# Optimization experiments

Measured on AMD Instinct MI355X. Metric: run time of the kernel, lower is better.

The kernel has to match this reference:

```python
import jax, jax.numpy as jnp
import numpy as np

NS = 50000   # sentence (src) nodes, unit==1
NW = 50000   # word (dst) nodes, unit==0
E = 1600000  # sw edges
IN_DIM = 128
OUT_DIM = 64


def setup_inputs() -> dict:
    key = jax.random.key(0)
    k1, k2, k3, k4, k5, k6 = jax.random.split(key, 6)
    return {
        "h": jax.random.normal(k1, (NS, IN_DIM), dtype=jnp.float32),
        "W_fc": jax.random.normal(k2, (IN_DIM, OUT_DIM), dtype=jnp.float32) * 0.05,
        "w_attn": jax.random.normal(k3, (2 * OUT_DIM, 1), dtype=jnp.float32) * 0.05,
        "weight": jax.random.uniform(k4, (E,), dtype=jnp.float32),
        "src_idx": jax.random.randint(k5, (E,), 0, NS, dtype=jnp.int32),
        "dst_idx": jax.random.randint(k6, (E,), 0, NW, dtype=jnp.int32),
    }


def reference(h, W_fc, w_attn, weight, src_idx, dst_idx):
    # z = fc(h) on source (sentence) nodes only; dst (word) nodes have z == 0 in DGL
    z = h @ W_fc                                   # [NS, OUT_DIM]
    zs = z[src_idx]                                # [E, OUT_DIM] gather src features
    # attn_fc(cat(z_src, z_dst)) with z_dst == 0 -> only first half of w_attn acts
    wa_src = w_attn[:OUT_DIM, 0]                   # [OUT_DIM]
    e = jax.nn.leaky_relu(zs @ wa_src)             # [E], slope 0.01 (torch default)
    e = weight * e                                 # tfidf edge weight scaling
    # edge-softmax per destination node (segment softmax over ragged mailbox)
    m = jax.ops.segment_max(e, dst_idx, num_segments=NW)          # [NW]
    m = jnp.where(jnp.isfinite(m), m, 0.0)                        # empty nodes
    ex = jnp.exp(e - m[dst_idx])                                  # [E]
    den = jax.ops.segment_sum(ex, dst_idx, num_segments=NW)       # [NW]
    alpha = ex / jnp.where(den == 0.0, 1.0, den)[dst_idx]         # [E]
    # weighted scatter-sum of neighbor features into dst nodes
    out = jax.ops.segment_sum(alpha[:, None] * zs, dst_idx, num_segments=NW)
    return out                                     # [NW, OUT_DIM]
```

## Files before the change

### kernel.cpp

```cpp
#include <hip/hip_runtime.h>
#include <hip/hip_fp16.h>
#include <math.h>

#define NS_ 50000
#define NW_ 50000
#define IN_DIM_ 128
#define OUT_DIM_ 64

#define NSLAB 512
#define NB 1563
#define CAPS 1280
#define CAPP 2304

typedef _Float16 h16x8 __attribute__((ext_vector_type(8)));
typedef float f32x4 __attribute__((ext_vector_type(4)));

__device__ inline float leaky01(float x) { return x > 0.0f ? x : 0.01f * x; }

__global__ __launch_bounds__(256) void prep_kernel(const float* __restrict__ Wfc,
                                                   const float* __restrict__ w_attn,
                                                   __half* __restrict__ W16f,
                                                   float* __restrict__ wv128) {
    int tid = threadIdx.x;
    for (int i = tid; i < IN_DIM_ * OUT_DIM_; i += 256) {
        int k = i >> 6, c = i & 63;
        int ni = c >> 4, c16 = c & 15, kstep = k >> 5, ks = (k & 31) >> 3, el = k & 7;
        W16f[(((ni * 4 + kstep) * 64) + ks * 16 + c16) * 8 + el] = __float2half(Wfc[i]);
    }
    if (tid < IN_DIM_) {
        float s = 0.f;
        for (int c = 0; c < OUT_DIM_; ++c) s += Wfc[tid * OUT_DIM_ + c] * w_attn[c];
        wv128[tid] = s;
    }
}

__global__ __launch_bounds__(256) void fc_kernel(const float* __restrict__ h,
                                                 const __half* __restrict__ W16f,
                                                 const float* __restrict__ wv128,
                                                 __half* __restrict__ z16,
                                                 float* __restrict__ t) {
    __shared__ __align__(16) __half Afrag[8192];
    __shared__ float ztile[64][68];
    int tid = threadIdx.x;
    int lane = tid & 63;
    int wv = tid >> 6;
    int row0 = blockIdx.x * 64;

    int k0 = (tid & 31) * 4;
    float4 wvv = *(const float4*)(wv128 + k0);
    int kstep = k0 >> 5, ks = (k0 & 31) >> 3, el = k0 & 7;
#pragma unroll
    for (int iter = 0; iter < 8; ++iter) {
        int r = (tid >> 5) + iter * 8;
        int row = row0 + r;
        float4 hv = (row < NS_) ? *(const float4*)(h + (size_t)row * IN_DIM_ + k0)
                                : make_float4(0.f, 0.f, 0.f, 0.f);
        int slot = ((r >> 4) * 4 + kstep) * 64 + ks * 16 + (r & 15);
        int slw = slot ^ ((slot >> 4) & 7);
        __half2 lo = __floats2half2_rn(hv.x, hv.y);
        __half2 hi = __floats2half2_rn(hv.z, hv.w);
        uint2 pk = make_uint2(*(unsigned*)&lo, *(unsigned*)&hi);
        *(uint2*)(&Afrag[slw * 8 + el]) = pk;
        float pt = hv.x * wvv.x + hv.y * wvv.y + hv.z * wvv.z + hv.w * wvv.w;
        pt += __shfl_down(pt, 16, 64);
        pt += __shfl_down(pt, 8, 64);
        pt += __shfl_down(pt, 4, 64);
        pt += __shfl_down(pt, 2, 64);
        pt += __shfl_down(pt, 1, 64);
        if ((tid & 31) == 0 && row < NS_) t[row] = pt;
    }
    __syncthreads();

    h16x8 af[4];
#pragma unroll
    for (int kst = 0; kst < 4; ++kst) {
        int s = (wv * 4 + kst) * 64 + lane;
        int sr = s ^ ((s >> 4) & 7);
        af[kst] = *(const h16x8*)(&Afrag[sr * 8]);
    }
#pragma unroll
    for (int ni = 0; ni < 4; ++ni) {
        f32x4 acc = {0.f, 0.f, 0.f, 0.f};
#pragma unroll
        for (int kst = 0; kst < 4; ++kst) {
            h16x8 bf = *(const h16x8*)(W16f + ((size_t)(ni * 4 + kst) * 64 + lane) * 8);
            acc = __builtin_amdgcn_mfma_f32_16x16x32_f16(af[kst], bf, acc, 0, 0, 0);
        }
        int col = ni * 16 + (lane & 15);
        int rb = wv * 16 + (lane >> 4) * 4;
        ztile[rb + 0][col] = acc[0];
        ztile[rb + 1][col] = acc[1];
        ztile[rb + 2][col] = acc[2];
        ztile[rb + 3][col] = acc[3];
    }
    __syncthreads();

    int nrows = NS_ - row0; if (nrows > 64) nrows = 64;
    for (int j = tid; j < 64 * 32; j += 256) {
        int r = j >> 5, c0 = (j & 31) * 2;
        if (r < nrows) {
            __half2 hp = __floats2half2_rn(ztile[r][c0], ztile[r][c0 + 1]);
            *(__half2*)(z16 + (size_t)(row0 + r) * OUT_DIM_ + c0) = hp;
        }
    }
}

__global__ __launch_bounds__(1024) void partition_kernel(const float* __restrict__ weight,
                                                         const int* __restrict__ src,
                                                         const int* __restrict__ dst,
                                                         const float* __restrict__ t,
                                                         unsigned* __restrict__ meta_sb,
                                                         int2* __restrict__ edata,
                                                         int E, int slab_e) {
    __shared__ int hist[NB];
    __shared__ int cur[NB];
    __shared__ int wsum[16];
    int tid = threadIdx.x;
    int lane = tid & 63;
    int wv = tid >> 6;
    int s = blockIdx.x;
    int e0 = s * slab_e;
    int e1 = e0 + slab_e; if (e1 > E) e1 = E;
    int cnt = e1 - e0;

    for (int i = tid; i < NB; i += 1024) hist[i] = 0;
    __syncthreads();

    float exr0 = 0, exr1 = 0, exr2 = 0, exr3 = 0;
    int mr0 = 0, mr1 = 0, mr2 = 0, mr3 = 0;
#define PART_LOAD(P, EXR, MR)                                              \
    {                                                                      \
        int i = tid + (P) * 1024;                                          \
        if (i < cnt) {                                                     \
            int e = e0 + i;                                                \
            int sr = src[e];                                               \
            int d = dst[e];                                                \
            float ev = weight[e] * leaky01(t[sr]);                         \
            EXR = __expf(ev);                                              \
            MR = sr | ((d & 31) << 16) | ((d >> 5) << 21);                 \
            atomicAdd(&hist[d >> 5], 1);                                   \
        }                                                                  \
    }
    PART_LOAD(0, exr0, mr0)
    PART_LOAD(1, exr1, mr1)
    PART_LOAD(2, exr2, mr2)
    PART_LOAD(3, exr3, mr3)
#undef PART_LOAD
    __syncthreads();

    int i0 = 2 * tid, i1 = 2 * tid + 1;
    int h0 = (i0 < NB) ? hist[i0] : 0;
    int h1 = (i1 < NB) ? hist[i1] : 0;
    int pairv = h0 + h1;
    int incl = pairv;
#pragma unroll
    for (int off = 1; off < 64; off <<= 1) {
        int u = __shfl_up(incl, off, 64);
        if (lane >= off) incl += u;
    }
    if (lane == 63) wsum[wv] = incl;
    __syncthreads();
    int woff = 0;
    for (int w = 0; w < wv; ++w) woff += wsum[w];
    incl += woff;
    int base = incl - pairv;
    if (i0 < NB) {
        cur[i0] = base;
        meta_sb[(size_t)s * NB + i0] = ((unsigned)h0 << 16) | (unsigned)base;
    }
    if (i1 < NB) {
        int b1 = base + h0;
        cur[i1] = b1;
        meta_sb[(size_t)s * NB + i1] = ((unsigned)h1 << 16) | (unsigned)b1;
    }
    __syncthreads();

#define PART_STORE(P, EXR, MR)                                             \
    {                                                                      \
        int i = tid + (P) * 1024;                                          \
        if (i < cnt) {                                                     \
            int b = ((unsigned)MR) >> 21;                                  \
            int pos = atomicAdd(&cur[b], 1);                               \
            edata[e0 + pos] = make_int2(__float_as_int(EXR), MR & 0x1FFFFF); \
        }                                                                  \
    }
    PART_STORE(0, exr0, mr0)
    PART_STORE(1, exr1, mr1)
    PART_STORE(2, exr2, mr2)
    PART_STORE(3, exr3, mr3)
#undef PART_STORE
}

__global__ __launch_bounds__(256) void meta_transpose_kernel(const unsigned* __restrict__ meta,
                                                             unsigned* __restrict__ metaT) {
    __shared__ unsigned tile[64][65];
    int b0 = blockIdx.x * 64;
    int s0 = blockIdx.y * 64;
    int tx = threadIdx.x & 63, ty = threadIdx.x >> 6;
    for (int r = ty; r < 64; r += 4) {
        int b = b0 + tx;
        tile[r][tx] = (b < NB) ? meta[(size_t)(s0 + r) * NB + b] : 0u;
    }
    __syncthreads();
    for (int r = ty; r < 64; r += 4) {
        int b = b0 + r;
        if (b < NB) metaT[(size_t)b * NSLAB + s0 + tx] = tile[tx][r];
    }
}

__global__ __launch_bounds__(512) void aggregate_kernel(const unsigned* __restrict__ metaT,
                                                        const int2* __restrict__ edata,
                                                        const __half* __restrict__ z16,
                                                        float* __restrict__ out,
                                                        int slab_e) {
    __shared__ int2 sbuf[CAPS];
    __shared__ int2 sorted[CAPP];
    __shared__ unsigned short soff[NSLAB];
    __shared__ int arr[NSLAB + 1];
    __shared__ int wsum[8];
    __shared__ float dden[32];
    __shared__ int dcnt[32];
    __shared__ int dbase[33];

    int orig = blockIdx.x;
    {
        const int nwg = NB, nx = 8;
        int q = nwg / nx, r = nwg % nx;
        int xcd = orig % nx, idx = orig / nx;
        orig = (xcd < r) ? xcd * (q + 1) + idx : r * (q + 1) + (xcd - r) * q + idx;
    }
    int b = orig;
    int tid = threadIdx.x;
    int lane = tid & 63;
    int wv = tid >> 6;

    int cntv;
    {
        unsigned mv = metaT[(size_t)b * NSLAB + tid];
        soff[tid] = (unsigned short)(mv & 0xFFFFu);
        cntv = (int)(mv >> 16);
    }
    if (tid < 32) { dden[tid] = 0.0f; dcnt[tid] = 0; }
    for (int i = tid; i < CAPP; i += 512) sorted[i] = make_int2(0, 0);

    int incl = cntv;
#pragma unroll
    for (int off = 1; off < 64; off <<= 1) {
        int u = __shfl_up(incl, off, 64);
        if (lane >= off) incl += u;
    }
    if (lane == 63) wsum[wv] = incl;
    __syncthreads();
    int woff = 0;
    for (int w = 0; w < wv; ++w) woff += wsum[w];
    incl += woff;
    arr[tid + 1] = incl;
    if (tid == 0) arr[0] = 0;
    __syncthreads();

    int total = arr[NSLAB];
    if (total > CAPS) total = CAPS;

    int gid = tid >> 1, l2 = tid & 1;
    for (int s = gid; s < NSLAB; s += 256) {
        int base = arr[s];
        int len = arr[s + 1] - base;
        int so = (int)soff[s];
        for (int j = l2; j < len; j += 2) {
            int p = base + j;
            if (p < CAPS) {
                int2 e = edata[(size_t)s * slab_e + so + j];
                sbuf[p] = e;
                int d5 = (e.y >> 16) & 31;
                atomicAdd(&dcnt[d5], 1);
                atomicAdd(&dden[d5], __int_as_float(e.x));
            }
        }
    }
    __syncthreads();

    if (tid < 32) {
        int v = dcnt[tid];
        int pv = (v + 31) & ~31;
        int iv = pv;
#pragma unroll
        for (int off = 1; off < 32; off <<= 1) {
            int u = __shfl_up(iv, off, 64);
            if (tid >= off) iv += u;
        }
        dbase[tid + 1] = iv;
        dcnt[tid] = iv - pv;
        if (tid == 0) dbase[0] = 0;
    }
    __syncthreads();

    for (int k = tid; k < total; k += 512) {
        int2 e = sbuf[k];
        int d5 = (e.y >> 16) & 31;
        int pos = atomicAdd(&dcnt[d5], 1);
        if (pos < CAPP) sorted[pos] = e;
    }
    __syncthreads();

    int qg = lane >> 4;
    int dl = lane & 15;
    const unsigned short* z16u = (const unsigned short*)z16;
    for (int q = 0; q < 4; ++q) {
        int d5 = wv * 4 + q;
        int d = b * 32 + d5;
        if (d >= NW_) continue;
        int a0 = dbase[d5];
        int npad = dbase[d5 + 1] - a0;
        float dn = dden[d5];
        float invdn = (dn > 0.0f) ? 1.0f / dn : 0.0f;
        float c0 = 0.f, c1 = 0.f, c2 = 0.f, c3 = 0.f;
        for (int j = 0; j < npad; j += 32) {
            int2 ee[8];
#pragma unroll
            for (int u = 0; u < 8; ++u) ee[u] = sorted[a0 + j + u * 4 + qg];
            uint2 zz[8];
#pragma unroll
            for (int u = 0; u < 8; ++u) {
                int srcr = ee[u].y & 0xFFFF;
                zz[u] = *(const uint2*)(z16u + (size_t)srcr * 64 + dl * 4);
            }
#pragma unroll
            for (int u = 0; u < 8; ++u) {
                float ex = __int_as_float(ee[u].x);
                __half2 p0 = *(__half2*)&zz[u].x;
                __half2 p1 = *(__half2*)&zz[u].y;
                c0 = fmaf(ex, __low2float(p0), c0);
                c1 = fmaf(ex, __high2float(p0), c1);
                c2 = fmaf(ex, __low2float(p1), c2);
                c3 = fmaf(ex, __high2float(p1), c3);
            }
        }
        c0 += __shfl_xor(c0, 16, 64); c1 += __shfl_xor(c1, 16, 64);
        c2 += __shfl_xor(c2, 16, 64); c3 += __shfl_xor(c3, 16, 64);
        c0 += __shfl_xor(c0, 32, 64); c1 += __shfl_xor(c1, 32, 64);
        c2 += __shfl_xor(c2, 32, 64); c3 += __shfl_xor(c3, 32, 64);
        if (lane < 16) {
            float4 st = make_float4(c0 * invdn, c1 * invdn, c2 * invdn, c3 * invdn);
            *(float4*)(out + (size_t)d * OUT_DIM_ + lane * 4) = st;
        }
    }
}

extern "C" void kernel_launch(void* const* d_in, const int* in_sizes, int n_in,
                              void* d_out, int out_size, void* d_ws, size_t ws_size,
                              hipStream_t stream) {
    const float* h      = (const float*)d_in[0];
    const float* Wfc    = (const float*)d_in[1];
    const float* w_attn = (const float*)d_in[2];
    const float* weight = (const float*)d_in[3];
    const int*   src    = (const int*)d_in[4];
    const int*   dst    = (const int*)d_in[5];
    int E = in_sizes[3];
    float* out = (float*)d_out;

    int slab_e = (E + NSLAB - 1) / NSLAB;

    int2*     edata = (int2*)d_ws;
    __half*   z16   = (__half*)(edata + (size_t)E);
    float*    t     = (float*)(z16 + (size_t)NS_ * OUT_DIM_);
    unsigned* meta  = (unsigned*)(t + NS_);
    unsigned* metaT = meta + (size_t)NSLAB * NB;
    __half*   W16f  = (__half*)(metaT + (size_t)NSLAB * NB);
    float*    wv128 = (float*)(W16f + 8192);

    prep_kernel<<<1, 256, 0, stream>>>(Wfc, w_attn, W16f, wv128);

    fc_kernel<<<(NS_ + 63) / 64, 256, 0, stream>>>(h, W16f, wv128, z16, t);

    partition_kernel<<<NSLAB, 1024, 0, stream>>>(weight, src, dst, t, meta, edata, E, slab_e);

    dim3 tg((NB + 63) / 64, NSLAB / 64);
    meta_transpose_kernel<<<tg, 256, 0, stream>>>(meta, metaT);

    aggregate_kernel<<<NB, 512, 0, stream>>>(metaT, edata, z16, out, slab_e);
}
```

Before: 85.24 us.

## Replace meta transpose with global column scan and compaction pass for contiguous buckets

Partition now accumulates per-bucket totals with global atomics. A new column-scan kernel computes global bucket starts and per-slab offsets, and a compact kernel copies each slab's bucket segments into a globally contiguous edge array. Aggregate then reads one contiguous range per bucket instead of gathering 512 small slab fragments with an in-block prefix scan. This costs an extra full pass over the edge data (read and write), plus a memset and two more launches.

```diff
diff --git a/kernel.cpp b/kernel.cpp
--- a/kernel.cpp
+++ b/kernel.cpp
@@ -110,6 +110,7 @@
                                                          const int* __restrict__ dst,
                                                          const float* __restrict__ t,
                                                          unsigned* __restrict__ meta_sb,
+                                                         int* __restrict__ btot,
                                                          int2* __restrict__ edata,
                                                          int E, int slab_e) {
     __shared__ int hist[NB];
@@ -167,11 +168,13 @@
     if (i0 < NB) {
         cur[i0] = base;
         meta_sb[(size_t)s * NB + i0] = ((unsigned)h0 << 16) | (unsigned)base;
+        if (h0 > 0) atomicAdd(&btot[i0], h0);
     }
     if (i1 < NB) {
         int b1 = base + h0;
         cur[i1] = b1;
         meta_sb[(size_t)s * NB + i1] = ((unsigned)h1 << 16) | (unsigned)b1;
+        if (h1 > 0) atomicAdd(&btot[i1], h1);
     }
     __syncthreads();
 
@@ -191,33 +194,94 @@
 #undef PART_STORE
 }
 
-__global__ __launch_bounds__(256) void meta_transpose_kernel(const unsigned* __restrict__ meta,
-                                                             unsigned* __restrict__ metaT) {
-    __shared__ unsigned tile[64][65];
+__global__ __launch_bounds__(512) void colscan_kernel(const unsigned* __restrict__ meta_sb,
+                                                      const int* __restrict__ btot,
+                                                      unsigned* __restrict__ gsub,
+                                                      int* __restrict__ bstart) {
+    __shared__ int wpart[8][64];
+    __shared__ int wred[8];
+    __shared__ int bst[64];
     int b0 = blockIdx.x * 64;
-    int s0 = blockIdx.y * 64;
-    int tx = threadIdx.x & 63, ty = threadIdx.x >> 6;
-    for (int r = ty; r < 64; r += 4) {
-        int b = b0 + tx;
-        tile[r][tx] = (b < NB) ? meta[(size_t)(s0 + r) * NB + b] : 0u;
-    }
-    __syncthreads();
-    for (int r = ty; r < 64; r += 4) {
-        int b = b0 + r;
-        if (b < NB) metaT[(size_t)b * NSLAB + s0 + tx] = tile[tx][r];
-    }
-}
-
-__global__ __launch_bounds__(512) void aggregate_kernel(const unsigned* __restrict__ metaT,
-                                                        const int2* __restrict__ edata,
+    int tid = threadIdx.x, lane = tid & 63, w = tid >> 6;
+    int nb = NB - b0; if (nb > 64) nb = 64;
+
+    int part = 0;
+    for (int i = tid; i < b0; i += 512) part += btot[i];
+#pragma unroll
+    for (int off = 32; off > 0; off >>= 1) part += __shfl_down(part, off, 64);
+    if (lane == 0) wred[w] = part;
+    __syncthreads();
+    if (tid == 0) {
+        int s_ = 0;
+        for (int i = 0; i < 8; ++i) s_ += wred[i];
+        wred[0] = s_;
+    }
+    __syncthreads();
+    int baseS = wred[0];
+
+    if (w == 0) {
+        int v = (lane < nb) ? btot[b0 + lane] : 0;
+        int incl = v;
+#pragma unroll
+        for (int off = 1; off < 64; off <<= 1) {
+            int u = __shfl_up(incl, off, 64);
+            if (lane >= off) incl += u;
+        }
+        if (lane < nb) {
+            int ex = baseS + incl - v;
+            bst[lane] = ex;
+            bstart[b0 + lane] = ex;
+            if (b0 + lane == NB - 1) bstart[NB] = baseS + incl;
+        }
+    }
+    __syncthreads();
+
+    int j = lane;
+    int csum = 0;
+    if (j < nb) {
+        for (int s = w * 64; s < w * 64 + 64; ++s)
+            csum += (int)(meta_sb[(size_t)s * NB + b0 + j] >> 16);
+    }
+    wpart[w][lane] = csum;
+    __syncthreads();
+    if (j < nb) {
+        int run = bst[j];
+        for (int w2 = 0; w2 < w; ++w2) run += wpart[w2][j];
+#pragma unroll 4
+        for (int s = w * 64; s < w * 64 + 64; ++s) {
+            unsigned mv = meta_sb[(size_t)s * NB + b0 + j];
+            gsub[(size_t)s * NB + b0 + j] = (unsigned)run;
+            run += (int)(mv >> 16);
+        }
+    }
+}
+
+__global__ __launch_bounds__(512) void compact_kernel(const unsigned* __restrict__ meta_sb,
+                                                      const unsigned* __restrict__ gsub,
+                                                      const int2* __restrict__ edata,
+                                                      int2* __restrict__ edata2,
+                                                      int slab_e) {
+    int s = blockIdx.x;
+    s = (s & 7) * 64 + (s >> 3);
+    int tid = threadIdx.x;
+    int e0 = s * slab_e;
+    for (int b = tid; b < NB; b += 512) {
+        unsigned mv = meta_sb[(size_t)s * NB + b];
+        int off = (int)(mv & 0xFFFFu);
+        int cnt = (int)(mv >> 16);
+        unsigned g = gsub[(size_t)s * NB + b];
+        const int2* sp = edata + e0 + off;
+        int2* dp = edata2 + g;
+        for (int i = 0; i < cnt; ++i) dp[i] = sp[i];
+    }
+}
+
+__global__ __launch_bounds__(512) void aggregate_kernel(const int* __restrict__ bstart,
+                                                        const int2* __restrict__ edata2,
                                                         const __half* __restrict__ z16,
-                                                        float* __restrict__ out,
-                                                        int slab_e) {
+                                                        float* __restrict__ out) {
     __shared__ int2 sbuf[CAPS];
     __shared__ int2 sorted[CAPP];
-    __shared__ unsigned short soff[NSLAB];
-    __shared__ int arr[NSLAB + 1];
-    __shared__ int wsum[8];
     __shared__ float dden[32];
     __shared__ int dcnt[32];
     __shared__ int dbase[33];
@@ -234,48 +298,20 @@
     int lane = tid & 63;
     int wv = tid >> 6;
 
-    int cntv;
-    {
-        unsigned mv = metaT[(size_t)b * NSLAB + tid];
-        soff[tid] = (unsigned short)(mv & 0xFFFFu);
-        cntv = (int)(mv >> 16);
-    }
+    int g0 = bstart[b];
+    int n = bstart[b + 1] - g0;
+    if (n > CAPS) n = CAPS;
+
     if (tid < 32) { dden[tid] = 0.0f; dcnt[tid] = 0; }
     for (int i = tid; i < CAPP; i += 512) sorted[i] = make_int2(0, 0);
-
-    int incl = cntv;
-#pragma unroll
-    for (int off = 1; off < 64; off <<= 1) {
-        int u = __shfl_up(incl, off, 64);
-        if (lane >= off) incl += u;
-    }
-    if (lane == 63) wsum[wv] = incl;
-    __syncthreads();
-    int woff = 0;
-    for (int w = 0; w < wv; ++w) woff += wsum[w];
-    incl += woff;
-    arr[tid + 1] = incl;
-    if (tid == 0) arr[0] = 0;
-    __syncthreads();
-
-    int total = arr[NSLAB];
-    if (total > CAPS) total = CAPS;
-
-    int gid = tid >> 1, l2 = tid & 1;
-    for (int s = gid; s < NSLAB; s += 256) {
-        int base = arr[s];
-        int len = arr[s + 1] - base;
-        int so = (int)soff[s];
-        for (int j = l2; j < len; j += 2) {
-            int p = base + j;
-            if (p < CAPS) {
-                int2 e = edata[(size_t)s * slab_e + so + j];
-                sbuf[p] = e;
-                int d5 = (e.y >> 16) & 31;
-                atomicAdd(&dcnt[d5], 1);
-                atomicAdd(&dden[d5], __int_as_float(e.x));
-            }
-        }
+    __syncthreads();
+
+    for (int k = tid; k < n; k += 512) {
+        int2 e = edata2[g0 + k];
+        sbuf[k] = e;
+        int d5 = (e.y >> 16) & 31;
+        atomicAdd(&dcnt[d5], 1);
+        atomicAdd(&dden[d5], __int_as_float(e.x));
     }
     __syncthreads();
 
@@ -294,7 +330,7 @@
     }
     __syncthreads();
 
-    for (int k = tid; k < total; k += 512) {
+    for (int k = tid; k < n; k += 512) {
         int2 e = sbuf[k];
         int d5 = (e.y >> 16) & 31;
         int pos = atomicAdd(&dcnt[d5], 1);
@@ -360,22 +396,28 @@
 
     int slab_e = (E + NSLAB - 1) / NSLAB;
 
-    int2*     edata = (int2*)d_ws;
-    __half*   z16   = (__half*)(edata + (size_t)E);
-    float*    t     = (float*)(z16 + (size_t)NS_ * OUT_DIM_);
-    unsigned* meta  = (unsigned*)(t + NS_);
-    unsigned* metaT = meta + (size_t)NSLAB * NB;
-    __half*   W16f  = (__half*)(metaT + (size_t)NSLAB * NB);
-    float*    wv128 = (float*)(W16f + 8192);
+    int2*     edata  = (int2*)d_ws;
+    int2*     edata2 = edata + (size_t)E;
+    __half*   z16    = (__half*)(edata2 + (size_t)E);
+    float*    t      = (float*)(z16 + (size_t)NS_ * OUT_DIM_);
+    unsigned* meta   = (unsigned*)(t + NS_);
+    unsigned* gsub   = meta + (size_t)NSLAB * NB;
+    int*      btot   = (int*)(gsub + (size_t)NSLAB * NB);
+    int*      bstart = btot + NB;
+    __half*   W16f   = (__half*)(bstart + NB + 1);
+    float*    wv128  = (float*)(W16f + 8192);
+
+    hipMemsetAsync(btot, 0, (size_t)NB * sizeof(int), stream);
 
     prep_kernel<<<1, 256, 0, stream>>>(Wfc, w_attn, W16f, wv128);
 
     fc_kernel<<<(NS_ + 63) / 64, 256, 0, stream>>>(h, W16f, wv128, z16, t);
 
-    partition_kernel<<<NSLAB, 1024, 0, stream>>>(weight, src, dst, t, meta, edata, E, slab_e);
-
-    dim3 tg((NB + 63) / 64, NSLAB / 64);
-    meta_transpose_kernel<<<tg, 256, 0, stream>>>(meta, metaT);
-
-    aggregate_kernel<<<NB, 512, 0, stream>>>(metaT, edata, z16, out, slab_e);
-}
+    partition_kernel<<<NSLAB, 1024, 0, stream>>>(weight, src, dst, t, meta, btot, edata, E, slab_e);
+
+    colscan_kernel<<<(NB + 63) / 64, 512, 0, stream>>>(meta, btot, gsub, bstart);
+
+    compact_kernel<<<NSLAB, 512, 0, stream>>>(meta, gsub, edata, edata2, slab_e);
+
+    aggregate_kernel<<<NB, 512, 0, stream>>>(bstart, edata2, z16, out);
+}
```

Measured after the change: 128.4 us. +50.6%, slower.
